# Performance work log

Measured on AMD Instinct MI355X. Metric: run time of the kernel, lower is better.

Reference implementation:

```python
import jax, jax.numpy as jnp
import numpy as np
import math

B, S, D = 4, 2048, 1024
NUM_HEADS = 16
HEAD_DIM = D // NUM_HEADS


def setup_inputs() -> dict:
    key = jax.random.key(0)
    ks = jax.random.split(key, 6)
    scale = 1.0 / math.sqrt(D)
    batch = jax.random.normal(ks[0], (B, S, D), dtype=jnp.float32)
    w_query = jax.random.normal(ks[1], (D, D), dtype=jnp.float32) * scale
    w_key = jax.random.normal(ks[2], (D, D), dtype=jnp.float32) * scale
    w_value = jax.random.normal(ks[3], (D, D), dtype=jnp.float32) * scale
    out_w = jax.random.normal(ks[4], (D, D), dtype=jnp.float32) * scale
    out_b = jax.random.normal(ks[5], (D,), dtype=jnp.float32) * 0.01
    return {"batch": batch, "w_query": w_query, "w_key": w_key,
            "w_value": w_value, "out_w": out_w, "out_b": out_b}


def reference(batch, w_query, w_key, w_value, out_w, out_b):
    b, s, _ = batch.shape
    # QKV projections (Linear with no bias): x @ W^T, here weights stored as [D,D] applied as x@W
    q = (batch @ w_query).reshape(b, s, NUM_HEADS, HEAD_DIM)
    k = (batch @ w_key).reshape(b, s, NUM_HEADS, HEAD_DIM)
    v = (batch @ w_value).reshape(b, s, NUM_HEADS, HEAD_DIM)
    # scores: [b, h, s, s]
    scores = jnp.einsum('bqhd,bkhd->bhqk', q, k)
    causal = jnp.tril(jnp.ones((s, s), dtype=bool))
    scores = jnp.where(causal, scores, -jnp.inf)
    # original divides by sqrt(head_dim) AFTER masking (-inf stays -inf)
    weights = jax.nn.softmax(scores / math.sqrt(HEAD_DIM), axis=-1)
    # dropout_percent = 0 -> identity
    out = jnp.einsum('bhqk,bkhd->bqhd', weights, v).reshape(b, s, D)
    return out @ out_w + out_b
```

## Files before the change

kernel.cpp:

```cpp
#include <hip/hip_runtime.h>
#include <hip/hip_bf16.h>

#define S_LEN 2048
#define D_DIM 1024
#define NHEAD 16
#define HDIM  64
#define BATCH 4
#define MROWS (BATCH*S_LEN)

typedef short bf16x8 __attribute__((ext_vector_type(8)));
typedef float f32x4  __attribute__((ext_vector_type(4)));
typedef float f32x16 __attribute__((ext_vector_type(16)));
typedef unsigned short u16;

#if __has_builtin(__builtin_amdgcn_exp2f)
#define EXP2(x) __builtin_amdgcn_exp2f(x)
#else
#define EXP2(x) __expf((x) * 0.6931471805599453f)
#endif

#define BAR() asm volatile("s_barrier" ::: "memory")
#define WAITV0() asm volatile("s_waitcnt vmcnt(0)" ::: "memory")
#define QSCALE 0.1803368801111137f

__device__ inline u16 f2bf(float f) {
  union { float f; unsigned u; } v; v.f = f;
  unsigned r = v.u + 0x7fff + ((v.u >> 16) & 1);
  return (u16)(r >> 16);
}

__device__ inline unsigned cvtpk(float lo, float hi_) {
  unsigned d;
  asm("v_cvt_pk_bf16_f32 %0, %1, %2" : "=v"(d) : "v"(lo), "v"(hi_));
  return d;
}

__device__ inline void perm32swap(unsigned& a, unsigned& b) {
  asm volatile("v_permlane32_swap_b32 %0, %1" : "+v"(a), "+v"(b));
}

__device__ inline void gload_lds16(const void* g, void* l) {
  __builtin_amdgcn_global_load_lds(
      (const __attribute__((address_space(1))) void*)g,
      (__attribute__((address_space(3))) void*)l, 16, 0, 0);
}

__global__ void cvt_x_kernel(const float* __restrict__ x, u16* __restrict__ xb, int n4) {
  int i = blockIdx.x * 256 + threadIdx.x;
  if (i >= n4) return;
  float4 v = reinterpret_cast<const float4*>(x)[i];
  ushort4 o;
  o.x = f2bf(v.x); o.y = f2bf(v.y); o.z = f2bf(v.z); o.w = f2bf(v.w);
  reinterpret_cast<ushort4*>(xb)[i] = o;
}

__global__ void transpose_w4_kernel(const float* __restrict__ wq, const float* __restrict__ wk,
                                    const float* __restrict__ wv, const float* __restrict__ wo,
                                    u16* __restrict__ wqkvT, u16* __restrict__ woT) {
  __shared__ float t[32][33];
  int z = blockIdx.z;
  const float* w = (z == 0) ? wq : (z == 1) ? wk : (z == 2) ? wv : wo;
  u16* wt = (z < 3) ? (wqkvT + (size_t)z * 1024 * 1024) : woT;
  const float sc = (z == 0) ? QSCALE : 1.0f;
  int tx = threadIdx.x, ty = threadIdx.y;
  int n0 = blockIdx.x * 32, k0 = blockIdx.y * 32;
#pragma unroll
  for (int j = 0; j < 32; j += 8)
    t[ty + j][tx] = w[(size_t)(k0 + ty + j) * D_DIM + n0 + tx];
  __syncthreads();
#pragma unroll
  for (int j = 0; j < 32; j += 8)
    wt[(size_t)(n0 + ty + j) * D_DIM + k0 + tx] = f2bf(t[tx][ty + j] * sc);
}

__global__ __launch_bounds__(256) void gemm_qkv_kernel(
    const u16* __restrict__ A, const u16* __restrict__ Bt,
    u16* __restrict__ Qb, u16* __restrict__ KP, u16* __restrict__ VP) {
  __shared__ u16 lA[128 * 32];
  __shared__ u16 lB[128 * 32];
  const int tid = threadIdx.x, wid = tid >> 6, lane = tid & 63;
  const int bm = blockIdx.y, bn = blockIdx.x;
  const int fr = lane & 15, fq = lane >> 4;
  const int r0 = wid * 32;
  const int srow = lane >> 2, scol = (lane & 3) * 8;
  const u16* gA = A + (size_t)(bm * 128 + r0 + srow) * 1024 + scol;
  const u16* gB = Bt + (size_t)(bn * 128 + r0 + srow) * 1024 + scol;
  u16* lA0 = &lA[r0 * 32];
  u16* lB0 = &lB[r0 * 32];

  f32x4 acc[4][4] = {};
  const int wm = (wid >> 1) * 64, wn = (wid & 1) * 64;

  for (int k0 = 0; k0 < 1024; k0 += 32) {
    gload_lds16(gA + k0,             lA0);
    gload_lds16(gA + k0 + 16 * 1024, lA0 + 16 * 32);
    gload_lds16(gB + k0,             lB0);
    gload_lds16(gB + k0 + 16 * 1024, lB0 + 16 * 32);
    __syncthreads();
    bf16x8 fa[4], fb[4];
#pragma unroll
    for (int i = 0; i < 4; i++) {
      fa[i] = *(const bf16x8*)&lA[(wm + i * 16 + fr) * 32 + fq * 8];
      fb[i] = *(const bf16x8*)&lB[(wn + i * 16 + fr) * 32 + fq * 8];
    }
#pragma unroll
    for (int i = 0; i < 4; i++)
#pragma unroll
      for (int j = 0; j < 4; j++)
        acc[i][j] = __builtin_amdgcn_mfma_f32_16x16x32_bf16(fa[i], fb[j], acc[i][j], 0, 0, 0);
    __syncthreads();
  }

  const int col0 = bn * 128;
  if (col0 < 1024) {
#pragma unroll
    for (int i = 0; i < 4; i++)
#pragma unroll
      for (int j = 0; j < 4; j++)
#pragma unroll
        for (int r = 0; r < 4; r++) {
          int row = bm * 128 + wm + i * 16 + fq * 4 + r;
          int col = col0 + wn + j * 16 + fr;
          Qb[(size_t)row * 1024 + col] = f2bf(acc[i][j][r]);
        }
  } else if (col0 < 2048) {
#pragma unroll
    for (int i = 0; i < 4; i++)
#pragma unroll
      for (int j = 0; j < 4; j++) {
        int col = col0 + wn + j * 16 + fr;
        int ck = col - 1024;
        int h = ck >> 6, d = ck & 63;
        int sfr = d >> 4, e = d & 7, hb = (d >> 3) & 1;
#pragma unroll
        for (int r = 0; r < 4; r++) {
          int row = bm * 128 + wm + i * 16 + fq * 4 + r;
          int b = row >> 11, sp = row & 2047;
          int bh = b * 16 + h, jt = sp >> 5;
          int lanep = (sp & 31) + 32 * hb;
          KP[((size_t)(bh * 64 + jt) * 4 + sfr) * 512 + lanep * 8 + e] = f2bf(acc[i][j][r]);
        }
      }
  } else {
#pragma unroll
    for (int i = 0; i < 4; i++)
#pragma unroll
      for (int j = 0; j < 4; j++) {
        int col = col0 + wn + j * 16 + fr;
        int cv = col - 2048;
        int h = cv >> 6, d = cv & 63;
        int R0 = bm * 128 + wm + i * 16 + fq * 4;
        int b = R0 >> 11, sp0 = R0 & 2047;
        int bh = b * 16 + h, jt = sp0 >> 5;
        int c = (d >> 5) * 2 + ((sp0 >> 4) & 1);
        int lanep = (d & 31) + 32 * ((sp0 >> 3) & 1);
        int e0 = sp0 & 7;
        ushort4 ov;
        ov.x = f2bf(acc[i][j][0]); ov.y = f2bf(acc[i][j][1]);
        ov.z = f2bf(acc[i][j][2]); ov.w = f2bf(acc[i][j][3]);
        *(ushort4*)(VP + ((size_t)(bh * 64 + jt) * 4 + c) * 512 + lanep * 8 + e0) = ov;
      }
  }
}

__global__ __launch_bounds__(256) void gemm_out_kernel(
    const u16* __restrict__ A, const u16* __restrict__ Bt,
    float* __restrict__ C, const float* __restrict__ bias) {
  __shared__ u16 lA[2][128 * 32];
  __shared__ u16 lB[2][128 * 32];
  const int tid = threadIdx.x, wid = tid >> 6, lane = tid & 63;
  const int bm = blockIdx.y, bn = blockIdx.x;
  const int fr = lane & 15, fq = lane >> 4;
  const int r0 = wid * 32;
  const int srow = lane >> 2, scol = (lane & 3) * 8;
  const u16* gA = A + (size_t)(bm * 128 + r0 + srow) * 1024 + scol;
  const u16* gB = Bt + (size_t)(bn * 128 + r0 + srow) * 1024 + scol;

  f32x4 acc[4][4] = {};
  const int wm = (wid >> 1) * 64, wn = (wid & 1) * 64;

  gload_lds16(gA,             &lA[0][r0 * 32]);
  gload_lds16(gA + 16 * 1024, &lA[0][r0 * 32 + 16 * 32]);
  gload_lds16(gB,             &lB[0][r0 * 32]);
  gload_lds16(gB + 16 * 1024, &lB[0][r0 * 32 + 16 * 32]);
  WAITV0();
  BAR();

#pragma unroll
  for (int k0 = 0; k0 < 1024; k0 += 32) {
    const int cur = (k0 >> 5) & 1, nxt = cur ^ 1;
    if (k0 + 32 < 1024) {
      gload_lds16(gA + k0 + 32,             &lA[nxt][r0 * 32]);
      gload_lds16(gA + k0 + 32 + 16 * 1024, &lA[nxt][r0 * 32 + 16 * 32]);
      gload_lds16(gB + k0 + 32,             &lB[nxt][r0 * 32]);
      gload_lds16(gB + k0 + 32 + 16 * 1024, &lB[nxt][r0 * 32 + 16 * 32]);
    }
    bf16x8 fa[4], fb[4];
#pragma unroll
    for (int i = 0; i < 4; i++) {
      fa[i] = *(const bf16x8*)&lA[cur][(wm + i * 16 + fr) * 32 + fq * 8];
      fb[i] = *(const bf16x8*)&lB[cur][(wn + i * 16 + fr) * 32 + fq * 8];
    }
#pragma unroll
    for (int i = 0; i < 4; i++)
#pragma unroll
      for (int j = 0; j < 4; j++)
        acc[i][j] = __builtin_amdgcn_mfma_f32_16x16x32_bf16(fa[i], fb[j], acc[i][j], 0, 0, 0);
    WAITV0();
    BAR();
  }

#pragma unroll
  for (int i = 0; i < 4; i++)
#pragma unroll
    for (int j = 0; j < 4; j++)
#pragma unroll
      for (int r = 0; r < 4; r++) {
        int row = bm * 128 + wm + i * 16 + fq * 4 + r;
        int col = bn * 128 + wn + j * 16 + fr;
        C[(size_t)row * 1024 + col] = acc[i][j][r] + bias[col];
      }
}

__global__ __launch_bounds__(256) void attn_kernel(
    const u16* __restrict__ Q, const u16* __restrict__ KP,
    const u16* __restrict__ VP, u16* __restrict__ O) {
  const int tid = threadIdx.x, wid = tid >> 6, lane = tid & 63;
  const int lq = lane & 31, hi = lane >> 5;
  int f = blockIdx.x;
  int xcd = f & 7, kk = f >> 3;
  int bh = xcd * 8 + (kk & 7);
  int qblk = 15 - (kk >> 3);
  int b = bh >> 4, h = bh & 15;
  int q0 = qblk * 128 + wid * 32;
  int q = q0 + lq;

  const u16* Qrow = Q + (size_t)(b * S_LEN + q) * D_DIM + h * HDIM;
  bf16x8 qf[4];
#pragma unroll
  for (int s = 0; s < 4; s++)
    qf[s] = *(const bf16x8*)(Qrow + s * 16 + hi * 8);

  const bf16x8* KPt = (const bf16x8*)KP + (size_t)bh * 64 * 4 * 64;
  const bf16x8* VPt = (const bf16x8*)VP + (size_t)bh * 64 * 4 * 64;

  f32x16 acc0 = {}, acc1 = {};
  float m = -3.0e38f, l = 0.f;
  const int nt = qblk * 4 + wid + 1;

  for (int t = 0; t < nt; ++t) {
    const int j0 = t * 32;
    const size_t fb = (size_t)t * 4 * 64 + lane;
    bf16x8 kf0 = KPt[fb], kf1 = KPt[fb + 64], kf2 = KPt[fb + 128], kf3 = KPt[fb + 192];
    bf16x8 vf00 = VPt[fb], vf01 = VPt[fb + 64], vf10 = VPt[fb + 128], vf11 = VPt[fb + 192];

    f32x16 sa = {};
    __builtin_amdgcn_s_setprio(1);
    sa = __builtin_amdgcn_mfma_f32_32x32x16_bf16(kf0, qf[0], sa, 0, 0, 0);
    sa = __builtin_amdgcn_mfma_f32_32x32x16_bf16(kf1, qf[1], sa, 0, 0, 0);
    sa = __builtin_amdgcn_mfma_f32_32x32x16_bf16(kf2, qf[2], sa, 0, 0, 0);
    sa = __builtin_amdgcn_mfma_f32_32x32x16_bf16(kf3, qf[3], sa, 0, 0, 0);
    __builtin_amdgcn_s_setprio(0);

    float p[16];
#pragma unroll
    for (int r = 0; r < 16; ++r) p[r] = sa[r];

    if (t == nt - 1) {
#pragma unroll
      for (int r = 0; r < 16; ++r) {
        int kidx = j0 + (r & 3) + 8 * (r >> 2) + 4 * hi;
        if (kidx > q) p[r] = -3.0e38f;
      }
    }

    float x8[8], x4[4], x2[2];
#pragma unroll
    for (int i = 0; i < 8; ++i) x8[i] = fmaxf(p[2 * i], p[2 * i + 1]);
#pragma unroll
    for (int i = 0; i < 4; ++i) x4[i] = fmaxf(x8[2 * i], x8[2 * i + 1]);
    x2[0] = fmaxf(x4[0], x4[1]); x2[1] = fmaxf(x4[2], x4[3]);
    float pm = fmaxf(x2[0], x2[1]);
    pm = fmaxf(pm, __shfl_xor(pm, 32));

    if (__any(pm > m + 11.5f)) {
      float mn = fmaxf(m, pm);
      float sc = EXP2(m - mn);
      l *= sc;
#pragma unroll
      for (int r = 0; r < 16; ++r) { acc0[r] *= sc; acc1[r] *= sc; }
      m = mn;
    }

    float rs = 0.f;
#pragma unroll
    for (int r = 0; r < 16; ++r) { p[r] = EXP2(p[r] - m); rs += p[r]; }
    rs += __shfl_xor(rs, 32);
    l += rs;

    unsigned c0 = cvtpk(p[0],  p[1]),  c1 = cvtpk(p[2],  p[3]);
    unsigned c2 = cvtpk(p[4],  p[5]),  c3 = cvtpk(p[6],  p[7]);
    unsigned c4 = cvtpk(p[8],  p[9]),  c5 = cvtpk(p[10], p[11]);
    unsigned c6 = cvtpk(p[12], p[13]), c7 = cvtpk(p[14], p[15]);
    perm32swap(c0, c2); perm32swap(c1, c3);
    perm32swap(c4, c6); perm32swap(c5, c7);
    union U4 { unsigned u[4]; bf16x8 v; } F0, F1;
    F0.u[0] = c0; F0.u[1] = c1; F0.u[2] = c2; F0.u[3] = c3;
    F1.u[0] = c4; F1.u[1] = c5; F1.u[2] = c6; F1.u[3] = c7;

    __builtin_amdgcn_s_setprio(1);
    acc0 = __builtin_amdgcn_mfma_f32_32x32x16_bf16(vf00, F0.v, acc0, 0, 0, 0);
    acc0 = __builtin_amdgcn_mfma_f32_32x32x16_bf16(vf01, F1.v, acc0, 0, 0, 0);
    acc1 = __builtin_amdgcn_mfma_f32_32x32x16_bf16(vf10, F0.v, acc1, 0, 0, 0);
    acc1 = __builtin_amdgcn_mfma_f32_32x32x16_bf16(vf11, F1.v, acc1, 0, 0, 0);
    __builtin_amdgcn_s_setprio(0);
  }

  float inv = 1.f / l;
  u16* Orow = O + (size_t)(b * S_LEN + q) * D_DIM + h * HDIM;
#pragma unroll
  for (int g = 0; g < 4; ++g) {
    ushort4 o4;
    o4.x = f2bf(acc0[g * 4 + 0] * inv);
    o4.y = f2bf(acc0[g * 4 + 1] * inv);
    o4.z = f2bf(acc0[g * 4 + 2] * inv);
    o4.w = f2bf(acc0[g * 4 + 3] * inv);
    *(ushort4*)(Orow + 8 * g + 4 * hi) = o4;
  }
#pragma unroll
  for (int g = 0; g < 4; ++g) {
    ushort4 o4;
    o4.x = f2bf(acc1[g * 4 + 0] * inv);
    o4.y = f2bf(acc1[g * 4 + 1] * inv);
    o4.z = f2bf(acc1[g * 4 + 2] * inv);
    o4.w = f2bf(acc1[g * 4 + 3] * inv);
    *(ushort4*)(Orow + 32 + 8 * g + 4 * hi) = o4;
  }
}

extern "C" void kernel_launch(void* const* d_in, const int* in_sizes, int n_in,
                              void* d_out, int out_size, void* d_ws, size_t ws_size,
                              hipStream_t stream) {
  const float* x  = (const float*)d_in[0];
  const float* wq = (const float*)d_in[1];
  const float* wk = (const float*)d_in[2];
  const float* wv = (const float*)d_in[3];
  const float* wo = (const float*)d_in[4];
  const float* ob = (const float*)d_in[5];
  float* out = (float*)d_out;

  char* ws = (char*)d_ws;
  u16* Xb    = (u16*)(ws);
  u16* Ab    = (u16*)(ws);
  u16* Qb    = (u16*)(ws + (size_t)16 * 1024 * 1024);
  u16* KPb   = (u16*)(ws + (size_t)32 * 1024 * 1024);
  u16* VPb   = (u16*)(ws + (size_t)48 * 1024 * 1024);
  u16* WqkvT = (u16*)(ws + (size_t)64 * 1024 * 1024);
  u16* WoT   = (u16*)(ws + (size_t)70 * 1024 * 1024);

  cvt_x_kernel<<<(MROWS * D_DIM / 4) / 256, 256, 0, stream>>>(x, Xb, MROWS * D_DIM / 4);

  transpose_w4_kernel<<<dim3(32, 32, 4), dim3(32, 8), 0, stream>>>(
      wq, wk, wv, wo, WqkvT, WoT);

  gemm_qkv_kernel<<<dim3(24, 64), 256, 0, stream>>>(Xb, WqkvT, Qb, KPb, VPb);

  attn_kernel<<<dim3(1024), 256, 0, stream>>>(Qb, KPb, VPb, Ab);

  gemm_out_kernel<<<dim3(8, 64), 256, 0, stream>>>(Ab, WoT, out, ob);
}
```

Measured before the change: 175.4 us.

## Pair low and high causal query blocks per workgroup to balance work and reuse K/V

Each attention workgroup now processes two query blocks, p and 15-p, so every block does the same number of causal tiles. K/V fragments loaded for the shared prefix are reused by both query sets, which halves K/V loads over that range. The grid drops from 1024 to 512 blocks. Per-wave register pressure rises with doubled Q fragments, accumulators and softmax state, which may cut occupancy.

```diff
diff --git a/kernel.cpp b/kernel.cpp
--- a/kernel.cpp
+++ b/kernel.cpp
@@ -222,6 +222,69 @@
       }
 }
 
+__device__ __forceinline__ void sm_pv(f32x16& sa, float& m, float& l,
+                                      f32x16& acc0, f32x16& acc1,
+                                      bf16x8 vf00, bf16x8 vf01,
+                                      bf16x8 vf10, bf16x8 vf11) {
+  float x8[8], x4[4];
+#pragma unroll
+  for (int i = 0; i < 8; ++i) x8[i] = fmaxf(sa[2 * i], sa[2 * i + 1]);
+#pragma unroll
+  for (int i = 0; i < 4; ++i) x4[i] = fmaxf(x8[2 * i], x8[2 * i + 1]);
+  float pm = fmaxf(fmaxf(x4[0], x4[1]), fmaxf(x4[2], x4[3]));
+  pm = fmaxf(pm, __shfl_xor(pm, 32));
+
+  if (__any(pm > m + 11.5f)) {
+    float mn = fmaxf(m, pm);
+    float sc = EXP2(m - mn);
+    l *= sc;
+#pragma unroll
+    for (int r = 0; r < 16; ++r) { acc0[r] *= sc; acc1[r] *= sc; }
+    m = mn;
+  }
+
+  float rs = 0.f;
+#pragma unroll
+  for (int r = 0; r < 16; ++r) { sa[r] = EXP2(sa[r] - m); rs += sa[r]; }
+  rs += __shfl_xor(rs, 32);
+  l += rs;
+
+  unsigned c0 = cvtpk(sa[0],  sa[1]),  c1 = cvtpk(sa[2],  sa[3]);
+  unsigned c2 = cvtpk(sa[4],  sa[5]),  c3 = cvtpk(sa[6],  sa[7]);
+  unsigned c4 = cvtpk(sa[8],  sa[9]),  c5 = cvtpk(sa[10], sa[11]);
+  unsigned c6 = cvtpk(sa[12], sa[13]), c7 = cvtpk(sa[14], sa[15]);
+  perm32swap(c0, c2); perm32swap(c1, c3);
+  perm32swap(c4, c6); perm32swap(c5, c7);
+  union U4 { unsigned u[4]; bf16x8 v; } F0, F1;
+  F0.u[0] = c0; F0.u[1] = c1; F0.u[2] = c2; F0.u[3] = c3;
+  F1.u[0] = c4; F1.u[1] = c5; F1.u[2] = c6; F1.u[3] = c7;
+
+  __builtin_amdgcn_s_setprio(1);
+  acc0 = __builtin_amdgcn_mfma_f32_32x32x16_bf16(vf00, F0.v, acc0, 0, 0, 0);
+  acc0 = __builtin_amdgcn_mfma_f32_32x32x16_bf16(vf01, F1.v, acc0, 0, 0, 0);
+  acc1 = __builtin_amdgcn_mfma_f32_32x32x16_bf16(vf10, F0.v, acc1, 0, 0, 0);
+  acc1 = __builtin_amdgcn_mfma_f32_32x32x16_bf16(vf11, F1.v, acc1, 0, 0, 0);
+  __builtin_amdgcn_s_setprio(0);
+}
+
+__device__ __forceinline__ void attn_store(u16* Orow, const f32x16& a0,
+                                           const f32x16& a1, float inv, int hi) {
+#pragma unroll
+  for (int g = 0; g < 4; ++g) {
+    ushort4 o4;
+    o4.x = f2bf(a0[g * 4 + 0] * inv); o4.y = f2bf(a0[g * 4 + 1] * inv);
+    o4.z = f2bf(a0[g * 4 + 2] * inv); o4.w = f2bf(a0[g * 4 + 3] * inv);
+    *(ushort4*)(Orow + 8 * g + 4 * hi) = o4;
+  }
+#pragma unroll
+  for (int g = 0; g < 4; ++g) {
+    ushort4 o4;
+    o4.x = f2bf(a1[g * 4 + 0] * inv); o4.y = f2bf(a1[g * 4 + 1] * inv);
+    o4.z = f2bf(a1[g * 4 + 2] * inv); o4.w = f2bf(a1[g * 4 + 3] * inv);
+    *(ushort4*)(Orow + 32 + 8 * g + 4 * hi) = o4;
+  }
+}
+
 __global__ __launch_bounds__(256) void attn_kernel(
     const u16* __restrict__ Q, const u16* __restrict__ KP,
     const u16* __restrict__ VP, u16* __restrict__ O) {
@@ -230,112 +293,83 @@
   int f = blockIdx.x;
   int xcd = f & 7, kk = f >> 3;
   int bh = xcd * 8 + (kk & 7);
-  int qblk = 15 - (kk >> 3);
+  int p  = kk >> 3;
   int b = bh >> 4, h = bh & 15;
-  int q0 = qblk * 128 + wid * 32;
-  int q = q0 + lq;
-
-  const u16* Qrow = Q + (size_t)(b * S_LEN + q) * D_DIM + h * HDIM;
-  bf16x8 qf[4];
-#pragma unroll
-  for (int s = 0; s < 4; s++)
-    qf[s] = *(const bf16x8*)(Qrow + s * 16 + hi * 8);
+  const int qL = p * 128 + wid * 32 + lq;
+  const int qH = (15 - p) * 128 + wid * 32 + lq;
+
+  const u16* QrowL = Q + (size_t)(b * S_LEN + qL) * D_DIM + h * HDIM;
+  const u16* QrowH = Q + (size_t)(b * S_LEN + qH) * D_DIM + h * HDIM;
+  bf16x8 qfL[4], qfH[4];
+#pragma unroll
+  for (int s = 0; s < 4; s++) {
+    qfL[s] = *(const bf16x8*)(QrowL + s * 16 + hi * 8);
+    qfH[s] = *(const bf16x8*)(QrowH + s * 16 + hi * 8);
+  }
 
   const bf16x8* KPt = (const bf16x8*)KP + (size_t)bh * 64 * 4 * 64;
   const bf16x8* VPt = (const bf16x8*)VP + (size_t)bh * 64 * 4 * 64;
 
-  f32x16 acc0 = {}, acc1 = {};
-  float m = -3.0e38f, l = 0.f;
-  const int nt = qblk * 4 + wid + 1;
-
-  for (int t = 0; t < nt; ++t) {
-    const int j0 = t * 32;
+  f32x16 aL0 = {}, aL1 = {}, aH0 = {}, aH1 = {};
+  float mL = -3.0e38f, lL = 0.f, mH = -3.0e38f, lH = 0.f;
+  const int ntL = 4 * p + wid + 1;
+  const int ntH = 60 - 4 * p + wid + 1;
+
+  for (int t = 0; t < ntL; ++t) {
     const size_t fb = (size_t)t * 4 * 64 + lane;
     bf16x8 kf0 = KPt[fb], kf1 = KPt[fb + 64], kf2 = KPt[fb + 128], kf3 = KPt[fb + 192];
     bf16x8 vf00 = VPt[fb], vf01 = VPt[fb + 64], vf10 = VPt[fb + 128], vf11 = VPt[fb + 192];
 
-    f32x16 sa = {};
+    f32x16 saL = {}, saH = {};
     __builtin_amdgcn_s_setprio(1);
-    sa = __builtin_amdgcn_mfma_f32_32x32x16_bf16(kf0, qf[0], sa, 0, 0, 0);
-    sa = __builtin_amdgcn_mfma_f32_32x32x16_bf16(kf1, qf[1], sa, 0, 0, 0);
-    sa = __builtin_amdgcn_mfma_f32_32x32x16_bf16(kf2, qf[2], sa, 0, 0, 0);
-    sa = __builtin_amdgcn_mfma_f32_32x32x16_bf16(kf3, qf[3], sa, 0, 0, 0);
+    saL = __builtin_amdgcn_mfma_f32_32x32x16_bf16(kf0, qfL[0], saL, 0, 0, 0);
+    saH = __builtin_amdgcn_mfma_f32_32x32x16_bf16(kf0, qfH[0], saH, 0, 0, 0);
+    saL = __builtin_amdgcn_mfma_f32_32x32x16_bf16(kf1, qfL[1], saL, 0, 0, 0);
+    saH = __builtin_amdgcn_mfma_f32_32x32x16_bf16(kf1, qfH[1], saH, 0, 0, 0);
+    saL = __builtin_amdgcn_mfma_f32_32x32x16_bf16(kf2, qfL[2], saL, 0, 0, 0);
+    saH = __builtin_amdgcn_mfma_f32_32x32x16_bf16(kf2, qfH[2], saH, 0, 0, 0);
+    saL = __builtin_amdgcn_mfma_f32_32x32x16_bf16(kf3, qfL[3], saL, 0, 0, 0);
+    saH = __builtin_amdgcn_mfma_f32_32x32x16_bf16(kf3, qfH[3], saH, 0, 0, 0);
     __builtin_amdgcn_s_setprio(0);
 
-    float p[16];
-#pragma unroll
-    for (int r = 0; r < 16; ++r) p[r] = sa[r];
-
-    if (t == nt - 1) {
+    if (t == ntL - 1) {
+      const int j0 = t * 32;
 #pragma unroll
       for (int r = 0; r < 16; ++r) {
         int kidx = j0 + (r & 3) + 8 * (r >> 2) + 4 * hi;
-        if (kidx > q) p[r] = -3.0e38f;
+        if (kidx > qL) saL[r] = -3.0e38f;
       }
     }
-
-    float x8[8], x4[4], x2[2];
-#pragma unroll
-    for (int i = 0; i < 8; ++i) x8[i] = fmaxf(p[2 * i], p[2 * i + 1]);
-#pragma unroll
-    for (int i = 0; i < 4; ++i) x4[i] = fmaxf(x8[2 * i], x8[2 * i + 1]);
-    x2[0] = fmaxf(x4[0], x4[1]); x2[1] = fmaxf(x4[2], x4[3]);
-    float pm = fmaxf(x2[0], x2[1]);
-    pm = fmaxf(pm, __shfl_xor(pm, 32));
-
-    if (__any(pm > m + 11.5f)) {
-      float mn = fmaxf(m, pm);
-      float sc = EXP2(m - mn);
-      l *= sc;
-#pragma unroll
-      for (int r = 0; r < 16; ++r) { acc0[r] *= sc; acc1[r] *= sc; }
-      m = mn;
+    sm_pv(saL, mL, lL, aL0, aL1, vf00, vf01, vf10, vf11);
+    sm_pv(saH, mH, lH, aH0, aH1, vf00, vf01, vf10, vf11);
+  }
+
+  for (int t = ntL; t < ntH; ++t) {
+    const size_t fb = (size_t)t * 4 * 64 + lane;
+    bf16x8 kf0 = KPt[fb], kf1 = KPt[fb + 64], kf2 = KPt[fb + 128], kf3 = KPt[fb + 192];
+    bf16x8 vf00 = VPt[fb], vf01 = VPt[fb + 64], vf10 = VPt[fb + 128], vf11 = VPt[fb + 192];
+
+    f32x16 saH = {};
+    __builtin_amdgcn_s_setprio(1);
+    saH = __builtin_amdgcn_mfma_f32_32x32x16_bf16(kf0, qfH[0], saH, 0, 0, 0);
+    saH = __builtin_amdgcn_mfma_f32_32x32x16_bf16(kf1, qfH[1], saH, 0, 0, 0);
+    saH = __builtin_amdgcn_mfma_f32_32x32x16_bf16(kf2, qfH[2], saH, 0, 0, 0);
+    saH = __builtin_amdgcn_mfma_f32_32x32x16_bf16(kf3, qfH[3], saH, 0, 0, 0);
+    __builtin_amdgcn_s_setprio(0);
+
+    if (t == ntH - 1) {
+      const int j0 = t * 32;
+#pragma unroll
+      for (int r = 0; r < 16; ++r) {
+        int kidx = j0 + (r & 3) + 8 * (r >> 2) + 4 * hi;
+        if (kidx > qH) saH[r] = -3.0e38f;
+      }
     }
-
-    float rs = 0.f;
-#pragma unroll
-    for (int r = 0; r < 16; ++r) { p[r] = EXP2(p[r] - m); rs += p[r]; }
-    rs += __shfl_xor(rs, 32);
-    l += rs;
-
-    unsigned c0 = cvtpk(p[0],  p[1]),  c1 = cvtpk(p[2],  p[3]);
-    unsigned c2 = cvtpk(p[4],  p[5]),  c3 = cvtpk(p[6],  p[7]);
-    unsigned c4 = cvtpk(p[8],  p[9]),  c5 = cvtpk(p[10], p[11]);
-    unsigned c6 = cvtpk(p[12], p[13]), c7 = cvtpk(p[14], p[15]);
-    perm32swap(c0, c2); perm32swap(c1, c3);
-    perm32swap(c4, c6); perm32swap(c5, c7);
-    union U4 { unsigned u[4]; bf16x8 v; } F0, F1;
-    F0.u[0] = c0; F0.u[1] = c1; F0.u[2] = c2; F0.u[3] = c3;
-    F1.u[0] = c4; F1.u[1] = c5; F1.u[2] = c6; F1.u[3] = c7;
-
-    __builtin_amdgcn_s_setprio(1);
-    acc0 = __builtin_amdgcn_mfma_f32_32x32x16_bf16(vf00, F0.v, acc0, 0, 0, 0);
-    acc0 = __builtin_amdgcn_mfma_f32_32x32x16_bf16(vf01, F1.v, acc0, 0, 0, 0);
-    acc1 = __builtin_amdgcn_mfma_f32_32x32x16_bf16(vf10, F0.v, acc1, 0, 0, 0);
-    acc1 = __builtin_amdgcn_mfma_f32_32x32x16_bf16(vf11, F1.v, acc1, 0, 0, 0);
-    __builtin_amdgcn_s_setprio(0);
-  }
-
-  float inv = 1.f / l;
-  u16* Orow = O + (size_t)(b * S_LEN + q) * D_DIM + h * HDIM;
-#pragma unroll
-  for (int g = 0; g < 4; ++g) {
-    ushort4 o4;
-    o4.x = f2bf(acc0[g * 4 + 0] * inv);
-    o4.y = f2bf(acc0[g * 4 + 1] * inv);
-    o4.z = f2bf(acc0[g * 4 + 2] * inv);
-    o4.w = f2bf(acc0[g * 4 + 3] * inv);
-    *(ushort4*)(Orow + 8 * g + 4 * hi) = o4;
-  }
-#pragma unroll
-  for (int g = 0; g < 4; ++g) {
-    ushort4 o4;
-    o4.x = f2bf(acc1[g * 4 + 0] * inv);
-    o4.y = f2bf(acc1[g * 4 + 1] * inv);
-    o4.z = f2bf(acc1[g * 4 + 2] * inv);
-    o4.w = f2bf(acc1[g * 4 + 3] * inv);
-    *(ushort4*)(Orow + 32 + 8 * g + 4 * hi) = o4;
-  }
+    sm_pv(saH, mH, lH, aH0, aH1, vf00, vf01, vf10, vf11);
+  }
+
+  attn_store(O + (size_t)(b * S_LEN + qL) * D_DIM + h * HDIM, aL0, aL1, 1.f / lL, hi);
+  attn_store(O + (size_t)(b * S_LEN + qH) * D_DIM + h * HDIM, aH0, aH1, 1.f / lH, hi);
 }
 
 extern "C" void kernel_launch(void* const* d_in, const int* in_sizes, int n_in,
@@ -365,7 +399,7 @@
 
   gemm_qkv_kernel<<<dim3(24, 64), 256, 0, stream>>>(Xb, WqkvT, Qb, KPb, VPb);
 
-  attn_kernel<<<dim3(1024), 256, 0, stream>>>(Qb, KPb, VPb, Ab);
+  attn_kernel<<<dim3(512), 256, 0, stream>>>(Qb, KPb, VPb, Ab);
 
   gemm_out_kernel<<<dim3(8, 64), 256, 0, stream>>>(Ab, WoT, out, ob);
 }
```

Result: slower. 202.9 us (+15.7%).
